# Kernel tuning notes

Measured on AMD Instinct MI355X. Metric: run time of the kernel, lower is better.

## Reference

```python
import jax, jax.numpy as jnp
import numpy as np
from jax import lax

STRIDE = 16
RATIOS = (0.5, 1.0, 2.0)
SCALES = (128.0, 256.0, 512.0)


def _anchor_template():
    # template[i] = [stride/2, stride/2, w, h], i = ri*3 + si
    r = jnp.asarray(RATIOS, jnp.float32)[:, None]        # (3,1)
    s = jnp.asarray(SCALES, jnp.float32)[None, :]        # (1,3)
    sqrt_r = jnp.sqrt(r)
    w = (s / sqrt_r)                                     # (3,3)
    h = (s * sqrt_r)
    half = jnp.full_like(w, STRIDE / 2.0)
    return jnp.stack([half, half, w, h], axis=-1).reshape(9, 4)  # (9,4) xywh


def setup_inputs() -> dict:
    key = jax.random.key(0)
    ks = jax.random.split(key, 6)
    B, C, H, W = 8, 512, 50, 76
    feature_maps = jax.random.normal(ks[0], (B, C, H, W), jnp.float32)
    conv_w = jax.random.normal(ks[1], (512, 512, 3, 3), jnp.float32) * 0.01
    conv_b = jnp.zeros((512,), jnp.float32)
    cls_w = jax.random.normal(ks[2], (18, 512, 1, 1), jnp.float32) * 0.01
    cls_b = jnp.zeros((18,), jnp.float32)
    reg_w = jax.random.normal(ks[3], (36, 512, 1, 1), jnp.float32) * 0.01
    reg_b = jnp.zeros((36,), jnp.float32)
    # (width, height) per image; x is clamped to im_size[0], y to im_size[1]
    img_size = jnp.tile(jnp.array([[W * STRIDE, H * STRIDE]], jnp.int32), (B, 1))
    return {"feature_maps": feature_maps, "conv_w": conv_w, "conv_b": conv_b,
            "cls_w": cls_w, "cls_b": cls_b, "reg_w": reg_w, "reg_b": reg_b,
            "img_size": img_size}


def reference(feature_maps, conv_w, conv_b, cls_w, cls_b, reg_w, reg_b, img_size):
    B, C, H, W = feature_maps.shape
    # 3x3 conv, pad=1, stride=1 + ReLU
    f = lax.conv_general_dilated(feature_maps, conv_w, (1, 1), 'SAME',
                                 dimension_numbers=('NCHW', 'OIHW', 'NCHW'))
    f = jax.nn.relu(f + conv_b[None, :, None, None])
    # 1x1 heads, then NCHW -> BHWC (matches the two torch transposes)
    cls = jnp.einsum('bchw,oc->bhwo', f, cls_w.reshape(18, 512)) + cls_b
    reg = jnp.einsum('bchw,oc->bhwo', f, reg_w.reshape(36, 512)) + reg_b
    cls = cls.reshape(B, H, W, 9, 2)
    reg = reg.reshape(B, H, W, 9, 4)

    # Vectorized anchor generation (replaces nested hi/wi loops)
    tmpl = _anchor_template()                              # (9,4)
    sx = (jnp.arange(W, dtype=jnp.float32) * STRIDE)[None, :]   # (1,W)
    sy = (jnp.arange(H, dtype=jnp.float32) * STRIDE)[:, None]   # (H,1)
    zeros = jnp.zeros((H, W), jnp.float32)
    shift = jnp.stack([jnp.broadcast_to(sx, (H, W)),
                       jnp.broadcast_to(sy, (H, W)), zeros, zeros], axis=-1)  # (H,W,4)
    anchors = tmpl[None, None] + shift[:, :, None, :]      # (H,W,9,4)
    anchors = jnp.broadcast_to(anchors, (B, H, W, 9, 4)).reshape(B, -1, 4)

    cls = cls.reshape(B, -1, 2)
    reg = reg.reshape(B, -1, 4)

    # anchor2bbox: inverse of the target encoding in loss()
    axy, awh = anchors[..., :2], anchors[..., 2:]
    pxy = axy + reg[..., :2] * awh
    pwh = awh * jnp.exp(reg[..., 2:])

    # eval-mode clip to image bounds (vectorized over batch)
    im = img_size.astype(jnp.float32)[:, None, :]          # (B,1,2) = (w,h)
    x1y1 = pxy - pwh / 2
    x2y2 = x1y1 + pwh
    x1y1 = jnp.clip(x1y1, 0.0, im)
    x2y2 = jnp.clip(x2y2, 0.0, im)
    wh = x2y2 - x1y1
    cxy = x1y1 + wh / 2
    proposals = jnp.concatenate([cxy, wh], axis=-1)        # (B, H*W*9, 4)
    return (proposals, cls)
```

## Files before the change

kernel.cpp:

```cpp
#include <hip/hip_runtime.h>

typedef __attribute__((ext_vector_type(8))) __bf16 bf16x8;
typedef __attribute__((ext_vector_type(4))) float  f32x4;

#define GPTR(p)   (__attribute__((address_space(1))) void*)(p)
#define LDSPTR(p) (__attribute__((address_space(3))) void*)(p)
#define MFMA16 __builtin_amdgcn_mfma_f32_16x16x32_bf16
#define PHB() do { __builtin_amdgcn_sched_barrier(0); __builtin_amdgcn_s_barrier(); __builtin_amdgcn_sched_barrier(0); } while (0)

__device__ __forceinline__ unsigned short f2bf(float f) {
    union { float f; unsigned u; } v; v.f = f;
    unsigned r = v.u + 0x7FFF + ((v.u >> 16) & 1);
    return (unsigned short)(r >> 16);
}

#define MTOT   30400
#define MPAD   30464
#define KTOT   4608
#define NT     72

__global__ __launch_bounds__(256) void pad_transpose(
    const float* __restrict__ in, unsigned short* __restrict__ P)
{
    __shared__ float t[32][33];
    const int tx = threadIdx.x;
    const int ty = threadIdx.y;
    const int tix = blockIdx.x % 3;
    const int cix = blockIdx.x / 3;
    const int y = blockIdx.y;
    const int b = blockIdx.z;
    const int x0 = tix * 32, c0 = cix * 32;

    const int x = x0 + tx;
    if (x < 76) {
#pragma unroll
        for (int i = 0; i < 4; ++i) {
            int c = c0 + ty + i * 8;
            t[ty + i * 8][tx] = in[((b * 512 + c) * 50 + y) * 76 + x];
        }
    }
    __syncthreads();
#pragma unroll
    for (int i = 0; i < 4; ++i) {
        int xr = ty + i * 8;
        int xw = x0 + xr;
        if (xw < 76) {
            P[((b * 52 + y + 1) * 78 + (xw + 1)) * 512 + c0 + tx] = f2bf(t[tx][xr]);
        }
    }
}

__global__ __launch_bounds__(256) void border_zero(unsigned short* __restrict__ P)
{
    int i = blockIdx.x * 256 + threadIdx.x;
    int b   = i >> 14;
    int rem = i & 16383;
    int seg = rem >> 6;
    int c8  = (rem & 63) << 3;
    int y, x;
    if (seg < 78)       { y = 0;  x = seg; }
    else if (seg < 156) { y = 51; x = seg - 78; }
    else if (seg < 206) { y = seg - 155; x = 0; }
    else                { y = seg - 205; x = 77; }
    *(float4*)(P + ((b * 52 + y) * 78 + x) * 512 + c8) = make_float4(0.f, 0.f, 0.f, 0.f);
}

__global__ __launch_bounds__(256) void wt_transform(
    const float* __restrict__ cw, unsigned short* __restrict__ Wt)
{
    int i = blockIdx.x * 256 + threadIdx.x;
    int o = i / KTOT;
    int r = i - o * KTOT;
    int kk = r >> 9;
    int c  = r & 511;
    Wt[i] = f2bf(cw[(o * 512 + c) * 9 + kk]);
}

__global__ __launch_bounds__(256) void head_wt(
    const float* __restrict__ cls_w, const float* __restrict__ reg_w,
    const float* __restrict__ cls_b, const float* __restrict__ reg_b,
    unsigned short* __restrict__ W2, float* __restrict__ b2)
{
    int i = blockIdx.x * 256 + threadIdx.x;
    int n = i >> 9, k = i & 511;
    float v = 0.f;
    if (n < 18) v = cls_w[n * 512 + k];
    else if (n < 54) v = reg_w[(n - 18) * 512 + k];
    W2[i] = f2bf(v);
    if (i < 64) {
        float bv = 0.f;
        if (i < 18) bv = cls_b[i];
        else if (i < 54) bv = reg_b[i - 18];
        b2[i] = bv;
    }
}

__global__ __launch_bounds__(512, 2) void conv_gemm8(
    const unsigned short* __restrict__ P,
    const unsigned short* __restrict__ Wt,
    const float* __restrict__ bias,
    unsigned short* __restrict__ F)
{
    __shared__ __attribute__((aligned(1024))) unsigned char lds[131072];

    const int tid = threadIdx.x;
    const int l   = tid & 63;
    const int w   = tid >> 6;
    const int wr  = w >> 2;
    const int nc  = w & 3;
    const int hB  = nc >> 1;
    const int rB  = (nc & 1) * 4;

    const int orig = blockIdx.y * 119 + blockIdx.x;
    const int xcd = orig & 7, seq = orig >> 3;
    const int wg  = (xcd < 6 ? xcd * 30 : 180 + (xcd - 6) * 29) + seq;
    const int m0  = (wg % 119) * 256;
    const int n0  = (wg / 119) * 256;

    const int loff = (l & 15) * 64 + (((l >> 4) * 16) ^ ((l & 8) ? 32 : 0));
    const int kelS = ((l & 3) * 8) ^ ((l & 32) ? 16 : 0);

    int cbA[2][2], nbB[2][2];
#pragma unroll
    for (int h = 0; h < 2; ++h)
#pragma unroll
        for (int j = 0; j < 2; ++j) {
            const int s    = j * 8 + w;
            const int rowt = h * 128 + (s >> 1) * 16 + (l >> 2);
            int m = m0 + rowt; if (m >= MTOT) m = 0;
            int b = m / 3800; int r = m - b * 3800;
            int y = r / 76;   int x = r - y * 76;
            cbA[h][j] = ((b * 52 + y + 1) * 78 + (x + 1)) * 512 + (s & 1) * 32 + kelS;
            nbB[h][j] = (n0 + rowt) * KTOT + (s & 1) * 32 + kelS;
        }

    auto stA = [&](int t, int h, unsigned char* abase) {
        const int kk  = t >> 3;
        const int tap = ((kk / 3 - 1) * 78 + (kk % 3 - 1)) * 512 + (t & 7) * 64;
#pragma unroll
        for (int j = 0; j < 2; ++j)
            __builtin_amdgcn_global_load_lds(GPTR(P + cbA[h][j] + tap),
                LDSPTR(abase + h * 16384 + j * 8192 + w * 1024), 16, 0, 0);
    };
    auto stB = [&](int t, int h, unsigned char* bbase) {
#pragma unroll
        for (int j = 0; j < 2; ++j)
            __builtin_amdgcn_global_load_lds(GPTR(Wt + nbB[h][j] + t * 64),
                LDSPTR(bbase + h * 16384 + j * 8192 + w * 1024), 16, 0, 0);
    };

    f32x4 acc[8][4];
#pragma unroll
    for (int i = 0; i < 8; ++i)
#pragma unroll
        for (int j = 0; j < 4; ++j) acc[i][j] = (f32x4){0.f, 0.f, 0.f, 0.f};

    {
        unsigned char* A0b = lds;
        unsigned char* B0b = lds + 32768;
        unsigned char* A1b = lds + 65536;
        unsigned char* B1b = lds + 65536 + 32768;
        stA(0, 0, A0b); stA(0, 1, A0b); stB(0, 0, B0b); stB(0, 1, B0b);
        stB(1, 0, B1b); stA(1, 0, A1b); stB(1, 1, B1b);
        __builtin_amdgcn_sched_barrier(0);
        asm volatile("s_waitcnt vmcnt(6)" ::: "memory");
        __builtin_amdgcn_s_barrier();
        __builtin_amdgcn_sched_barrier(0);
    }

#define RD(basep, subR, ks) (*(const bf16x8*)((basep) + (((subR) * 2 + (ks)) * 1024) + loff))

    for (int g = 0; g < NT; ++g) {
        unsigned char* Ac = lds + (g & 1) * 65536;
        unsigned char* Bc = Ac + 32768;
        unsigned char* An = lds + (((g & 1) ^ 1)) * 65536;
        unsigned char* Ah = Ac + wr * 16384;
        unsigned char* Bh = Bc + hB * 16384;

        bf16x8 a[4][2], bb0[2][2], bb1[2][2];

#pragma unroll
        for (int f = 0; f < 4; ++f)
#pragma unroll
            for (int ks = 0; ks < 2; ++ks) a[f][ks] = RD(Ah, f, ks);
#pragma unroll
        for (int ni = 0; ni < 2; ++ni)
#pragma unroll
            for (int ks = 0; ks < 2; ++ks) bb0[ni][ks] = RD(Bh, rB + ni, ks);
        if (g < NT - 1) stA(g + 1, 1, An);
        PHB();
        __builtin_amdgcn_s_setprio(1);
#pragma unroll
        for (int f = 0; f < 4; ++f)
#pragma unroll
            for (int ni = 0; ni < 2; ++ni)
#pragma unroll
                for (int ks = 0; ks < 2; ++ks)
                    acc[f][ni] = MFMA16(a[f][ks], bb0[ni][ks], acc[f][ni], 0, 0, 0);
        __builtin_amdgcn_s_setprio(0);
        PHB();

#pragma unroll
        for (int ni = 0; ni < 2; ++ni)
#pragma unroll
            for (int ks = 0; ks < 2; ++ks) bb1[ni][ks] = RD(Bh, rB + 2 + ni, ks);
        PHB();
        __builtin_amdgcn_s_setprio(1);
#pragma unroll
        for (int f = 0; f < 4; ++f)
#pragma unroll
            for (int ni = 0; ni < 2; ++ni)
#pragma unroll
                for (int ks = 0; ks < 2; ++ks)
                    acc[f][2 + ni] = MFMA16(a[f][ks], bb1[ni][ks], acc[f][2 + ni], 0, 0, 0);
        __builtin_amdgcn_s_setprio(0);
        PHB();

#pragma unroll
        for (int f = 0; f < 4; ++f)
#pragma unroll
            for (int ks = 0; ks < 2; ++ks) a[f][ks] = RD(Ah, 4 + f, ks);
        if (g < NT - 2) stB(g + 2, 0, Bc);
        PHB();
        __builtin_amdgcn_s_setprio(1);
#pragma unroll
        for (int f = 0; f < 4; ++f)
#pragma unroll
            for (int ni = 0; ni < 2; ++ni)
#pragma unroll
                for (int ks = 0; ks < 2; ++ks)
                    acc[4 + f][2 + ni] = MFMA16(a[f][ks], bb1[ni][ks], acc[4 + f][2 + ni], 0, 0, 0);
        __builtin_amdgcn_s_setprio(0);
        PHB();

        if (g < NT - 2) { stA(g + 2, 0, Ac); stB(g + 2, 1, Bc); }
        __builtin_amdgcn_s_setprio(1);
#pragma unroll
        for (int f = 0; f < 4; ++f)
#pragma unroll
            for (int ni = 0; ni < 2; ++ni)
#pragma unroll
                for (int ks = 0; ks < 2; ++ks)
                    acc[4 + f][ni] = MFMA16(a[f][ks], bb0[ni][ks], acc[4 + f][ni], 0, 0, 0);
        __builtin_amdgcn_s_setprio(0);
        __builtin_amdgcn_sched_barrier(0);
        if (g < NT - 2)       asm volatile("s_waitcnt vmcnt(6)" ::: "memory");
        else if (g == NT - 2) asm volatile("s_waitcnt vmcnt(0)" ::: "memory");
        __builtin_amdgcn_s_barrier();
        __builtin_amdgcn_sched_barrier(0);
    }
#undef RD

#pragma unroll
    for (int ni = 0; ni < 4; ++ni) {
        const int col = n0 + nc * 64 + ni * 16 + (l & 15);
        const float bcol = bias[col];
#pragma unroll
        for (int mi = 0; mi < 8; ++mi) {
#pragma unroll
            for (int jj = 0; jj < 4; ++jj) {
                const int row = m0 + wr * 128 + mi * 16 + (l >> 4) * 4 + jj;
                if (row < MTOT)
                    F[row * 512 + col] = f2bf(fmaxf(acc[mi][ni][jj] + bcol, 0.f));
            }
        }
    }
}

__global__ __launch_bounds__(256) void head_decode(
    const unsigned short* __restrict__ F,
    const unsigned short* __restrict__ W2,
    const float* __restrict__ b2,
    const int* __restrict__ img,
    float* __restrict__ out)
{
    __shared__ float S[64][56];
    const int tid  = threadIdx.x;
    const int lane = tid & 63;
    const int wv   = tid >> 6;
    const int mblk = blockIdx.x * 64;
    const int arow = mblk + wv * 16 + (lane & 15);

    f32x4 acc[4];
#pragma unroll
    for (int ni = 0; ni < 4; ++ni) acc[ni] = (f32x4){0.f, 0.f, 0.f, 0.f};

#pragma unroll 4
    for (int ks = 0; ks < 16; ++ks) {
        const int kloc = ks * 32 + (lane >> 4) * 8;
        bf16x8 a = *(const bf16x8*)(F + arow * 512 + kloc);
#pragma unroll
        for (int ni = 0; ni < 4; ++ni) {
            bf16x8 b = *(const bf16x8*)(W2 + (ni * 16 + (lane & 15)) * 512 + kloc);
            acc[ni] = MFMA16(a, b, acc[ni], 0, 0, 0);
        }
    }

#pragma unroll
    for (int ni = 0; ni < 4; ++ni) {
        int col = ni * 16 + (lane & 15);
        if (col < 54) {
            float bb = b2[col];
#pragma unroll
            for (int j = 0; j < 4; ++j)
                S[wv * 16 + (lane >> 4) * 4 + j][col] = acc[ni][j] + bb;
        }
    }
    __syncthreads();

    for (int it = tid; it < 576; it += 256) {
        int rowl = it / 9;
        int a    = it - rowl * 9;
        int m = mblk + rowl;
        if (m >= MTOT) continue;
        int b   = m / 3800;
        int rem = m - b * 3800;
        int y = rem / 76;
        int x = rem - y * 76;

        int ri = a / 3, si = a - ri * 3;
        float sqr = (ri == 0) ? 0.70710678118654752f : ((ri == 1) ? 1.f : 1.41421356237309515f);
        float scale = (float)(128 << si);
        float wa = scale / sqr;
        float ha = scale * sqr;
        float ax = (float)x * 16.f + 8.f;
        float ay = (float)y * 16.f + 8.f;

        float r0 = S[rowl][18 + a * 4 + 0];
        float r1 = S[rowl][18 + a * 4 + 1];
        float r2 = S[rowl][18 + a * 4 + 2];
        float r3 = S[rowl][18 + a * 4 + 3];

        float px = ax + r0 * wa;
        float py = ay + r1 * ha;
        float pw = wa * expf(r2);
        float ph = ha * expf(r3);

        float x1 = px - 0.5f * pw, y1 = py - 0.5f * ph;
        float x2 = x1 + pw,        y2 = y1 + ph;
        float imx = (float)img[2 * b], imy = (float)img[2 * b + 1];
        x1 = fminf(fmaxf(x1, 0.f), imx); x2 = fminf(fmaxf(x2, 0.f), imx);
        y1 = fminf(fmaxf(y1, 0.f), imy); y2 = fminf(fmaxf(y2, 0.f), imy);
        float ww = x2 - x1, hh = y2 - y1;
        float cx = x1 + 0.5f * ww, cy = y1 + 0.5f * hh;

        int pidx = b * 34200 + rem * 9 + a;
        ((float4*)out)[pidx] = make_float4(cx, cy, ww, hh);
        float* oc = out + 1094400 + pidx * 2;
        oc[0] = S[rowl][a * 2 + 0];
        oc[1] = S[rowl][a * 2 + 1];
    }
}

extern "C" void kernel_launch(void* const* d_in, const int* in_sizes, int n_in,
                              void* d_out, int out_size, void* d_ws, size_t ws_size,
                              hipStream_t stream) {
    const float* fm     = (const float*)d_in[0];
    const float* conv_w = (const float*)d_in[1];
    const float* conv_b = (const float*)d_in[2];
    const float* cls_w  = (const float*)d_in[3];
    const float* cls_b  = (const float*)d_in[4];
    const float* reg_w  = (const float*)d_in[5];
    const float* reg_b  = (const float*)d_in[6];
    const int*   img    = (const int*)d_in[7];
    float* out = (float*)d_out;

    char* ws = (char*)d_ws;
    unsigned short* P  = (unsigned short*)(ws);
    unsigned short* Wt = (unsigned short*)(ws + 33226752);
    unsigned short* F  = (unsigned short*)(ws + 37945344);
    unsigned short* W2 = (unsigned short*)(ws + 69140480);
    float*          b2 = (float*)(ws + 69206016);

    hipMemsetAsync((char*)F + (size_t)MTOT * 512 * 2, 0, (size_t)(MPAD - MTOT) * 512 * 2, stream);

    border_zero<<<512, 256, 0, stream>>>(P);
    pad_transpose<<<dim3(48, 50, 8), dim3(32, 8, 1), 0, stream>>>(fm, P);
    wt_transform<<<9216, 256, 0, stream>>>(conv_w, Wt);
    head_wt<<<128, 256, 0, stream>>>(cls_w, reg_w, cls_b, reg_b, W2, b2);
    conv_gemm8<<<dim3(119, 2), 512, 0, stream>>>(P, Wt, conv_b, F);
    head_decode<<<476, 256, 0, stream>>>(F, W2, b2, img, out);
}
```

Baseline: 201.3 us.

## Prefetch next tile's B fragments early and reorder loads in conv GEMM main loop

Restructures the implicit-GEMM conv main loop so the first B fragment set for the next K tile is read from LDS during the current tile, before the last MFMA phase. The loop is unrolled by two with ping-pong B registers, and the issue order of the global-to-LDS loads is changed to B before A. Waitcnt and barrier placement are adjusted to match. The aim is to hide LDS read latency at the tile boundary, at the cost of more registers and an extra barrier per tile.

```diff
diff --git a/kernel.cpp b/kernel.cpp
--- a/kernel.cpp
+++ b/kernel.cpp
@@ -6,7 +6,8 @@
 #define GPTR(p)   (__attribute__((address_space(1))) void*)(p)
 #define LDSPTR(p) (__attribute__((address_space(3))) void*)(p)
 #define MFMA16 __builtin_amdgcn_mfma_f32_16x16x32_bf16
-#define PHB() do { __builtin_amdgcn_sched_barrier(0); __builtin_amdgcn_s_barrier(); __builtin_amdgcn_sched_barrier(0); } while (0)
+#define SB() __builtin_amdgcn_sched_barrier(0)
+#define PHB() do { SB(); __builtin_amdgcn_s_barrier(); SB(); } while (0)
 
 __device__ __forceinline__ unsigned short f2bf(float f) {
     union { float f; unsigned u; } v; v.f = f;
@@ -155,100 +156,124 @@
 #pragma unroll
         for (int j = 0; j < 4; ++j) acc[i][j] = (f32x4){0.f, 0.f, 0.f, 0.f};
 
+#define RD(basep, subR, ks) (*(const bf16x8*)((basep) + (((subR) * 2 + (ks)) * 1024) + loff))
+
+    bf16x8 b0x[2][2], b0y[2][2];
+
     {
         unsigned char* A0b = lds;
         unsigned char* B0b = lds + 32768;
         unsigned char* A1b = lds + 65536;
         unsigned char* B1b = lds + 65536 + 32768;
-        stA(0, 0, A0b); stA(0, 1, A0b); stB(0, 0, B0b); stB(0, 1, B0b);
-        stB(1, 0, B1b); stA(1, 0, A1b); stB(1, 1, B1b);
-        __builtin_amdgcn_sched_barrier(0);
+        stB(0, 0, B0b); stB(0, 1, B0b); stA(0, 0, A0b); stA(0, 1, A0b);
+        stB(1, 0, B1b); stB(1, 1, B1b); stA(1, 0, A1b);
+        SB();
         asm volatile("s_waitcnt vmcnt(6)" ::: "memory");
         __builtin_amdgcn_s_barrier();
-        __builtin_amdgcn_sched_barrier(0);
-    }
-
-#define RD(basep, subR, ks) (*(const bf16x8*)((basep) + (((subR) * 2 + (ks)) * 1024) + loff))
-
-    for (int g = 0; g < NT; ++g) {
-        unsigned char* Ac = lds + (g & 1) * 65536;
-        unsigned char* Bc = Ac + 32768;
-        unsigned char* An = lds + (((g & 1) ^ 1)) * 65536;
-        unsigned char* Ah = Ac + wr * 16384;
-        unsigned char* Bh = Bc + hB * 16384;
-
-        bf16x8 a[4][2], bb0[2][2], bb1[2][2];
-
-#pragma unroll
-        for (int f = 0; f < 4; ++f)
-#pragma unroll
-            for (int ks = 0; ks < 2; ++ks) a[f][ks] = RD(Ah, f, ks);
+        SB();
 #pragma unroll
         for (int ni = 0; ni < 2; ++ni)
 #pragma unroll
-            for (int ks = 0; ks < 2; ++ks) bb0[ni][ks] = RD(Bh, rB + ni, ks);
-        if (g < NT - 1) stA(g + 1, 1, An);
-        PHB();
-        __builtin_amdgcn_s_setprio(1);
-#pragma unroll
-        for (int f = 0; f < 4; ++f)
-#pragma unroll
-            for (int ni = 0; ni < 2; ++ni)
-#pragma unroll
-                for (int ks = 0; ks < 2; ++ks)
-                    acc[f][ni] = MFMA16(a[f][ks], bb0[ni][ks], acc[f][ni], 0, 0, 0);
-        __builtin_amdgcn_s_setprio(0);
-        PHB();
-
-#pragma unroll
-        for (int ni = 0; ni < 2; ++ni)
-#pragma unroll
-            for (int ks = 0; ks < 2; ++ks) bb1[ni][ks] = RD(Bh, rB + 2 + ni, ks);
-        PHB();
-        __builtin_amdgcn_s_setprio(1);
-#pragma unroll
-        for (int f = 0; f < 4; ++f)
-#pragma unroll
-            for (int ni = 0; ni < 2; ++ni)
-#pragma unroll
-                for (int ks = 0; ks < 2; ++ks)
-                    acc[f][2 + ni] = MFMA16(a[f][ks], bb1[ni][ks], acc[f][2 + ni], 0, 0, 0);
-        __builtin_amdgcn_s_setprio(0);
-        PHB();
-
-#pragma unroll
-        for (int f = 0; f < 4; ++f)
-#pragma unroll
-            for (int ks = 0; ks < 2; ++ks) a[f][ks] = RD(Ah, 4 + f, ks);
-        if (g < NT - 2) stB(g + 2, 0, Bc);
-        PHB();
-        __builtin_amdgcn_s_setprio(1);
-#pragma unroll
-        for (int f = 0; f < 4; ++f)
-#pragma unroll
-            for (int ni = 0; ni < 2; ++ni)
-#pragma unroll
-                for (int ks = 0; ks < 2; ++ks)
-                    acc[4 + f][2 + ni] = MFMA16(a[f][ks], bb1[ni][ks], acc[4 + f][2 + ni], 0, 0, 0);
-        __builtin_amdgcn_s_setprio(0);
-        PHB();
-
-        if (g < NT - 2) { stA(g + 2, 0, Ac); stB(g + 2, 1, Bc); }
-        __builtin_amdgcn_s_setprio(1);
-#pragma unroll
-        for (int f = 0; f < 4; ++f)
-#pragma unroll
-            for (int ni = 0; ni < 2; ++ni)
-#pragma unroll
-                for (int ks = 0; ks < 2; ++ks)
-                    acc[4 + f][ni] = MFMA16(a[f][ks], bb0[ni][ks], acc[4 + f][ni], 0, 0, 0);
-        __builtin_amdgcn_s_setprio(0);
-        __builtin_amdgcn_sched_barrier(0);
-        if (g < NT - 2)       asm volatile("s_waitcnt vmcnt(6)" ::: "memory");
-        else if (g == NT - 2) asm volatile("s_waitcnt vmcnt(0)" ::: "memory");
-        __builtin_amdgcn_s_barrier();
-        __builtin_amdgcn_sched_barrier(0);
-    }
+            for (int ks = 0; ks < 2; ++ks)
+                b0x[ni][ks] = RD(B0b + hB * 16384, rB + ni, ks);
+    }
+
+#define TILE_BODY(G, B0C, B0N)                                                  \
+    {                                                                           \
+        const int gt = (G);                                                     \
+        unsigned char* Ac = lds + (gt & 1) * 65536;                             \
+        unsigned char* Bc = Ac + 32768;                                         \
+        unsigned char* An = lds + ((gt & 1) ^ 1) * 65536;                       \
+        unsigned char* Bn = An + 32768;                                         \
+        unsigned char* Ah = Ac + wr * 16384;                                    \
+        unsigned char* Bh = Bc + hB * 16384;                                    \
+        unsigned char* BhN = Bn + hB * 16384;                                   \
+        bf16x8 a[4][2], bb1[2][2];                                              \
+         \
+        _Pragma("unroll")                                                       \
+        for (int f = 0; f < 4; ++f)                                             \
+            _Pragma("unroll")                                                   \
+            for (int ks = 0; ks < 2; ++ks) a[f][ks] = RD(Ah, f, ks);            \
+        if (gt + 1 < NT) stA(gt + 1, 1, An);                                    \
+        PHB();                                                                  \
+        __builtin_amdgcn_s_setprio(1);                                          \
+        _Pragma("unroll")                                                       \
+        for (int f = 0; f < 4; ++f)                                             \
+            _Pragma("unroll")                                                   \
+            for (int ni = 0; ni < 2; ++ni)                                      \
+                _Pragma("unroll")                                               \
+                for (int ks = 0; ks < 2; ++ks)                                  \
+                    acc[f][ni] = MFMA16(a[f][ks], B0C[ni][ks], acc[f][ni], 0, 0, 0); \
+        __builtin_amdgcn_s_setprio(0);                                          \
+        PHB();                                                                  \
+                       \
+        _Pragma("unroll")                                                       \
+        for (int ni = 0; ni < 2; ++ni)                                          \
+            _Pragma("unroll")                                                   \
+            for (int ks = 0; ks < 2; ++ks) bb1[ni][ks] = RD(Bh, rB + 2 + ni, ks); \
+        PHB();                                                                  \
+        __builtin_amdgcn_s_setprio(1);                                          \
+        _Pragma("unroll")                                                       \
+        for (int f = 0; f < 4; ++f)                                             \
+            _Pragma("unroll")                                                   \
+            for (int ni = 0; ni < 2; ++ni)                                      \
+                _Pragma("unroll")                                               \
+                for (int ks = 0; ks < 2; ++ks)                                  \
+                    acc[f][2 + ni] = MFMA16(a[f][ks], bb1[ni][ks], acc[f][2 + ni], 0, 0, 0); \
+        __builtin_amdgcn_s_setprio(0);                                          \
+        PHB();                                                                  \
+                     \
+        _Pragma("unroll")                                                       \
+        for (int f = 0; f < 4; ++f)                                             \
+            _Pragma("unroll")                                                   \
+            for (int ks = 0; ks < 2; ++ks) a[f][ks] = RD(Ah, 4 + f, ks);        \
+        if (gt + 2 < NT) stB(gt + 2, 0, Bc);                                    \
+        PHB();                                                                  \
+        __builtin_amdgcn_s_setprio(1);                                          \
+        _Pragma("unroll")                                                       \
+        for (int f = 0; f < 4; ++f)                                             \
+            _Pragma("unroll")                                                   \
+            for (int ni = 0; ni < 2; ++ni)                                      \
+                _Pragma("unroll")                                               \
+                for (int ks = 0; ks < 2; ++ks)                                  \
+                    acc[4 + f][2 + ni] = MFMA16(a[f][ks], bb1[ni][ks], acc[4 + f][2 + ni], 0, 0, 0); \
+        __builtin_amdgcn_s_setprio(0);                                          \
+        SB();                                                                   \
+        if (gt + 2 < NT)      asm volatile("s_waitcnt vmcnt(6)" ::: "memory");  \
+        else if (gt + 1 < NT) asm volatile("s_waitcnt vmcnt(4)" ::: "memory");  \
+        __builtin_amdgcn_s_barrier();                                           \
+        SB();                                                                   \
+           \
+        if (gt + 1 < NT) {                                                      \
+            _Pragma("unroll")                                                   \
+            for (int ni = 0; ni < 2; ++ni)                                      \
+                _Pragma("unroll")                                               \
+                for (int ks = 0; ks < 2; ++ks)                                  \
+                    B0N[ni][ks] = RD(BhN, rB + ni, ks);                         \
+        }                                                                       \
+        if (gt + 2 < NT) { stB(gt + 2, 1, Bc); stA(gt + 2, 0, Ac); }            \
+        PHB();                                                                  \
+        __builtin_amdgcn_s_setprio(1);                                          \
+        _Pragma("unroll")                                                       \
+        for (int f = 0; f < 4; ++f)                                             \
+            _Pragma("unroll")                                                   \
+            for (int ni = 0; ni < 2; ++ni)                                      \
+                _Pragma("unroll")                                               \
+                for (int ks = 0; ks < 2; ++ks)                                  \
+                    acc[4 + f][ni] = MFMA16(a[f][ks], B0C[ni][ks], acc[4 + f][ni], 0, 0, 0); \
+        __builtin_amdgcn_s_setprio(0);                                          \
+        SB();                                                                   \
+        if (gt + 2 < NT)      asm volatile("s_waitcnt vmcnt(6)" ::: "memory");  \
+        else if (gt + 1 < NT) asm volatile("s_waitcnt vmcnt(0)" ::: "memory");  \
+        __builtin_amdgcn_s_barrier();                                           \
+        SB();                                                                   \
+    }
+
+    for (int g = 0; g < NT; g += 2) {
+        TILE_BODY(g,     b0x, b0y)
+        TILE_BODY(g + 1, b0y, b0x)
+    }
+#undef TILE_BODY
 #undef RD
 
 #pragma unroll
```

After: 199.3 us. About the same (-1.0%).

## Replace phased ping-pong GEMM schedule with simple one-ahead double buffering

Applied to the files above, without the earlier changes.

The conv GEMM main loop drops its phased schedule, which had intra-iteration barriers, s_setprio around MFMA bursts, partial vmcnt waits and prefetch two tiles ahead. Instead it issues all global-to-LDS loads for the next K tile at the top of each iteration, runs all four MFMA blocks with no barriers in between, and ends with a single __syncthreads. The aim is to cut barrier and scheduling overhead and let the compiler interleave LDS reads with MFMAs more freely. The cost is a shallower prefetch: the full barrier waits for every outstanding load each iteration, so global latency may be hidden less well.

```diff
diff --git a/kernel.cpp b/kernel.cpp
--- a/kernel.cpp
+++ b/kernel.cpp
@@ -6,7 +6,7 @@
 #define GPTR(p)   (__attribute__((address_space(1))) void*)(p)
 #define LDSPTR(p) (__attribute__((address_space(3))) void*)(p)
 #define MFMA16 __builtin_amdgcn_mfma_f32_16x16x32_bf16
-#define PHB() do { __builtin_amdgcn_sched_barrier(0); __builtin_amdgcn_s_barrier(); __builtin_amdgcn_sched_barrier(0); } while (0)
+#define SB() __builtin_amdgcn_sched_barrier(0)
 
 __device__ __forceinline__ unsigned short f2bf(float f) {
     union { float f; unsigned u; } v; v.f = f;
@@ -155,99 +155,80 @@
 #pragma unroll
         for (int j = 0; j < 4; ++j) acc[i][j] = (f32x4){0.f, 0.f, 0.f, 0.f};
 
+#define RD(basep, subR, ks) (*(const bf16x8*)((basep) + (((subR) * 2 + (ks)) * 1024) + loff))
+
     {
         unsigned char* A0b = lds;
         unsigned char* B0b = lds + 32768;
-        unsigned char* A1b = lds + 65536;
-        unsigned char* B1b = lds + 65536 + 32768;
-        stA(0, 0, A0b); stA(0, 1, A0b); stB(0, 0, B0b); stB(0, 1, B0b);
-        stB(1, 0, B1b); stA(1, 0, A1b); stB(1, 1, B1b);
-        __builtin_amdgcn_sched_barrier(0);
-        asm volatile("s_waitcnt vmcnt(6)" ::: "memory");
-        __builtin_amdgcn_s_barrier();
-        __builtin_amdgcn_sched_barrier(0);
-    }
-
-#define RD(basep, subR, ks) (*(const bf16x8*)((basep) + (((subR) * 2 + (ks)) * 1024) + loff))
+        stB(0, 0, B0b); stB(0, 1, B0b); stA(0, 0, A0b); stA(0, 1, A0b);
+        __syncthreads();
+    }
 
     for (int g = 0; g < NT; ++g) {
         unsigned char* Ac = lds + (g & 1) * 65536;
         unsigned char* Bc = Ac + 32768;
         unsigned char* An = lds + (((g & 1) ^ 1)) * 65536;
+        unsigned char* Bn = An + 32768;
         unsigned char* Ah = Ac + wr * 16384;
         unsigned char* Bh = Bc + hB * 16384;
 
-        bf16x8 a[4][2], bb0[2][2], bb1[2][2];
-
-#pragma unroll
-        for (int f = 0; f < 4; ++f)
-#pragma unroll
-            for (int ks = 0; ks < 2; ++ks) a[f][ks] = RD(Ah, f, ks);
+        if (g + 1 < NT) {
+            stB(g + 1, 0, Bn); stB(g + 1, 1, Bn);
+            stA(g + 1, 0, An); stA(g + 1, 1, An);
+        }
+        SB();
+
+        bf16x8 a0[4][2], a1[4][2], b0[2][2], b1[2][2];
+
+#pragma unroll
+        for (int f = 0; f < 4; ++f)
+#pragma unroll
+            for (int ks = 0; ks < 2; ++ks) a0[f][ks] = RD(Ah, f, ks);
 #pragma unroll
         for (int ni = 0; ni < 2; ++ni)
 #pragma unroll
-            for (int ks = 0; ks < 2; ++ks) bb0[ni][ks] = RD(Bh, rB + ni, ks);
-        if (g < NT - 1) stA(g + 1, 1, An);
-        PHB();
-        __builtin_amdgcn_s_setprio(1);
+            for (int ks = 0; ks < 2; ++ks) b0[ni][ks] = RD(Bh, rB + ni, ks);
 #pragma unroll
         for (int f = 0; f < 4; ++f)
 #pragma unroll
             for (int ni = 0; ni < 2; ++ni)
 #pragma unroll
                 for (int ks = 0; ks < 2; ++ks)
-                    acc[f][ni] = MFMA16(a[f][ks], bb0[ni][ks], acc[f][ni], 0, 0, 0);
-        __builtin_amdgcn_s_setprio(0);
-        PHB();
+                    acc[f][ni] = MFMA16(a0[f][ks], b0[ni][ks], acc[f][ni], 0, 0, 0);
 
 #pragma unroll
         for (int ni = 0; ni < 2; ++ni)
 #pragma unroll
-            for (int ks = 0; ks < 2; ++ks) bb1[ni][ks] = RD(Bh, rB + 2 + ni, ks);
-        PHB();
-        __builtin_amdgcn_s_setprio(1);
+            for (int ks = 0; ks < 2; ++ks) b1[ni][ks] = RD(Bh, rB + 2 + ni, ks);
 #pragma unroll
         for (int f = 0; f < 4; ++f)
 #pragma unroll
             for (int ni = 0; ni < 2; ++ni)
 #pragma unroll
                 for (int ks = 0; ks < 2; ++ks)
-                    acc[f][2 + ni] = MFMA16(a[f][ks], bb1[ni][ks], acc[f][2 + ni], 0, 0, 0);
-        __builtin_amdgcn_s_setprio(0);
-        PHB();
-
-#pragma unroll
-        for (int f = 0; f < 4; ++f)
-#pragma unroll
-            for (int ks = 0; ks < 2; ++ks) a[f][ks] = RD(Ah, 4 + f, ks);
-        if (g < NT - 2) stB(g + 2, 0, Bc);
-        PHB();
-        __builtin_amdgcn_s_setprio(1);
+                    acc[f][2 + ni] = MFMA16(a0[f][ks], b1[ni][ks], acc[f][2 + ni], 0, 0, 0);
+
+#pragma unroll
+        for (int f = 0; f < 4; ++f)
+#pragma unroll
+            for (int ks = 0; ks < 2; ++ks) a1[f][ks] = RD(Ah, 4 + f, ks);
 #pragma unroll
         for (int f = 0; f < 4; ++f)
 #pragma unroll
             for (int ni = 0; ni < 2; ++ni)
 #pragma unroll
                 for (int ks = 0; ks < 2; ++ks)
-                    acc[4 + f][2 + ni] = MFMA16(a[f][ks], bb1[ni][ks], acc[4 + f][2 + ni], 0, 0, 0);
-        __builtin_amdgcn_s_setprio(0);
-        PHB();
-
-        if (g < NT - 2) { stA(g + 2, 0, Ac); stB(g + 2, 1, Bc); }
-        __builtin_amdgcn_s_setprio(1);
+                    acc[4 + f][2 + ni] = MFMA16(a1[f][ks], b1[ni][ks], acc[4 + f][2 + ni], 0, 0, 0);
+
 #pragma unroll
         for (int f = 0; f < 4; ++f)
 #pragma unroll
             for (int ni = 0; ni < 2; ++ni)
 #pragma unroll
                 for (int ks = 0; ks < 2; ++ks)
-                    acc[4 + f][ni] = MFMA16(a[f][ks], bb0[ni][ks], acc[4 + f][ni], 0, 0, 0);
-        __builtin_amdgcn_s_setprio(0);
-        __builtin_amdgcn_sched_barrier(0);
-        if (g < NT - 2)       asm volatile("s_waitcnt vmcnt(6)" ::: "memory");
-        else if (g == NT - 2) asm volatile("s_waitcnt vmcnt(0)" ::: "memory");
-        __builtin_amdgcn_s_barrier();
-        __builtin_amdgcn_sched_barrier(0);
+                    acc[4 + f][ni] = MFMA16(a1[f][ks], b0[ni][ks], acc[4 + f][ni], 0, 0, 0);
+
+        __syncthreads();
     }
 #undef RD
 
```

New measurement: 205.0 us. No clear change (+1.9%).
